# Kernel tuning notes

Measured on AMD Instinct MI355X. Metric: run time of the kernel, lower is better.

The kernel has to match this reference:

```python
import jax, jax.numpy as jnp
import numpy as np

E, K, H, I = 8, 2, 768, 1152  # experts, top_k, hidden, intermediate
T = 4096  # total tokens


def setup_inputs() -> dict:
    key = jax.random.key(0)
    ks = jax.random.split(key, 6)
    return {
        "x": jax.random.normal(ks[0], (T, H), jnp.float32),
        "gate_w": jax.random.normal(ks[1], (E, H), jnp.float32) * 0.02,
        "correction_bias": jnp.zeros((E,), jnp.float32),
        "Wi": jax.random.normal(ks[2], (E, H, 2 * I), jnp.float32) * 0.02,
        "Wo": jax.random.normal(ks[3], (E, I, H), jnp.float32) * 0.02,
        "shared_Wi": jax.random.normal(ks[4], (2 * I, H), jnp.float32) * 0.02,
        "shared_Wo": jax.random.normal(ks[5], (H, I), jnp.float32) * 0.02,
    }


def reference(x, gate_w, correction_bias, Wi, Wo, shared_Wi, shared_Wo):
    # ---- shared SwiGLU expert (dropout=0 in eval) ----
    sh = x @ shared_Wi.T                      # (T, 2I)
    s_in, s_gate = sh[:, :I], sh[:, I:]
    shared_out = (jax.nn.silu(s_in) * s_gate) @ shared_Wo.T  # (T, H)

    # ---- sigmoid top-k router with bias correction ----
    logits = jax.nn.sigmoid(x @ gate_w.T)     # (T, E)
    sel = logits + correction_bias
    _, indices = jax.lax.top_k(sel, K)        # (T, K)
    weights = jnp.take_along_axis(logits, indices, axis=-1)  # bias-free scores
    weights = weights / jnp.sum(weights, axis=-1, keepdims=True)

    # combine weight per (expert, token): cw[e, t] = sum_k weights[t,k]*[indices[t,k]==e]
    one_hot = jax.nn.one_hot(indices, E, dtype=x.dtype)      # (T, K, E)
    cw = jnp.einsum("tke,tk->et", one_hot, weights)          # (E, T)

    # ---- experts: SwiGLU per expert, weighted scatter-combine ----
    h = jnp.einsum("th,ehf->etf", x, Wi)      # (E, T, 2I)
    proj, gate = h[..., :I], h[..., I:]
    act = jax.nn.silu(gate) * proj            # (E, T, I)
    act = act * cw[:, :, None]                # fold combine weights before Wo
    expert_out = jnp.einsum("eti,eih->th", act, Wo)          # (T, H)

    return expert_out + shared_out
```

## Files before the change

### kernel.cpp

```cpp
#include <hip/hip_runtime.h>
#include <stdint.h>

#define E_  8
#define H_  768
#define I_  1152
#define T_  4096
#define F2_ (2*I_)
#define RBMAX 104

typedef unsigned short u16;
typedef __attribute__((ext_vector_type(8))) __bf16 bf16x8;
typedef __attribute__((ext_vector_type(8))) unsigned short u16x8;
typedef __attribute__((ext_vector_type(4))) float floatx4;

typedef const void __attribute__((address_space(1))) as1_void;
typedef void __attribute__((address_space(3))) as3_void;

__device__ __forceinline__ void gld16(void* lds, const void* g) {
  __builtin_amdgcn_global_load_lds((as1_void*)g, (as3_void*)lds, 16, 0, 0);
}

__device__ __forceinline__ u16 f2bf(float f) {
  union { float f; unsigned int i; } v; v.f = f;
  unsigned int r = v.i + 0x7FFF + ((v.i >> 16) & 1);
  return (u16)(r >> 16);
}


__device__ __forceinline__ void pack_direct(const float* __restrict__ src,
                                            u16* __restrict__ dst, int N, int K,
                                            int n0, int k0, int tid) {
  int n = tid & 63, kc2 = tid >> 6;
  int KT = K >> 5;
  #pragma unroll
  for (int pass = 0; pass < 2; pass++) {
    int kc = kc2 + pass * 4;
    int k  = k0 + kc * 8;
    const float* sp = src + (long)(n0 + n) * K + k;
    float4 v0 = *(const float4*)sp;
    float4 v1 = *(const float4*)(sp + 4);
    u16x8 u;
    u[0]=f2bf(v0.x); u[1]=f2bf(v0.y); u[2]=f2bf(v0.z); u[3]=f2bf(v0.w);
    u[4]=f2bf(v1.x); u[5]=f2bf(v1.y); u[6]=f2bf(v1.z); u[7]=f2bf(v1.w);
    long p = (long)((n0 + n) >> 4) * KT + (k >> 5);
    int lane = (n & 15) | ((kc & 3) << 4);
    *(u16x8*)(dst + (p * 64 + lane) * 8) = u;
  }
}

__device__ __forceinline__ void pack_transpose(const float* __restrict__ src,
                                               u16* __restrict__ dst, int N, int K,
                                               int n0, int k0, float (*tile)[65], int tid) {
  int cc = tid & 63, rr = tid >> 6;
  #pragma unroll
  for (int p = 0; p < 16; p++)
    tile[rr + p * 4][cc] = src[(long)(k0 + rr + p * 4) * N + n0 + cc];
  __syncthreads();
  int n = tid & 63, kc2 = tid >> 6;
  int KT = K >> 5;
  #pragma unroll
  for (int pass = 0; pass < 2; pass++) {
    int kc = kc2 + pass * 4;
    int k  = k0 + kc * 8;
    u16x8 u;
    #pragma unroll
    for (int e = 0; e < 8; e++) u[e] = f2bf(tile[kc * 8 + e][n]);
    long p = (long)((n0 + n) >> 4) * KT + (k >> 5);
    int lane = (n & 15) | ((kc & 3) << 4);
    *(u16x8*)(dst + (p * 64 + lane) * 8) = u;
  }
}

__global__ void prep_kernel(const float* __restrict__ x, const float* __restrict__ gw,
                            const float* __restrict__ bias,
                            int* __restrict__ top2e, float* __restrict__ top2w,
                            u16* __restrict__ xb,
                            const float* __restrict__ sWi, u16* __restrict__ sWip,
                            const float* __restrict__ sWo, u16* __restrict__ sWop,
                            const float* __restrict__ Wi, u16* __restrict__ Wip,
                            const float* __restrict__ Wo, u16* __restrict__ Wop) {
  __shared__ float tile[64][65];
  int b = blockIdx.x, tid = threadIdx.x;
  if (b < 1024) {
    int t    = b * 4 + (tid >> 6);
    int lane = tid & 63;
    float acc[E_];
    #pragma unroll
    for (int e = 0; e < E_; e++) acc[e] = 0.f;
    #pragma unroll
    for (int i = 0; i < H_ / 256; i++) {
      int c = i * 256 + lane * 4;
      float4 xv = *(const float4*)(x + (long)t * H_ + c);
      ushort4 u;
      u.x = f2bf(xv.x); u.y = f2bf(xv.y); u.z = f2bf(xv.z); u.w = f2bf(xv.w);
      *(ushort4*)(xb + (long)t * H_ + c) = u;
      #pragma unroll
      for (int e = 0; e < E_; e++) {
        float4 g = *(const float4*)(gw + e * H_ + c);
        acc[e] += xv.x * g.x + xv.y * g.y + xv.z * g.z + xv.w * g.w;
      }
    }
    #pragma unroll
    for (int e = 0; e < E_; e++) {
      #pragma unroll
      for (int s = 32; s > 0; s >>= 1) acc[e] += __shfl_xor(acc[e], s);
    }
    if (lane == 0) {
      float logits[E_], sel[E_];
      #pragma unroll
      for (int e = 0; e < E_; e++) {
        logits[e] = 1.f / (1.f + expf(-acc[e]));
        sel[e]    = logits[e] + bias[e];
      }
      int i0 = 0;
      #pragma unroll
      for (int e = 1; e < E_; e++) if (sel[e] > sel[i0]) i0 = e;
      int i1 = (i0 == 0) ? 1 : 0;
      #pragma unroll
      for (int e = 0; e < E_; e++) if (e != i0 && sel[e] > sel[i1]) i1 = e;
      float w0 = logits[i0], w1 = logits[i1], s = w0 + w1;
      top2e[t * 2 + 0] = i0;  top2w[t * 2 + 0] = w0 / s;
      top2e[t * 2 + 1] = i1;  top2w[t * 2 + 1] = w1 / s;
    }
  } else if (b < 1456) {
    int idx = b - 1024;
    int bx = idx % 36, by = idx / 36;
    pack_direct(sWi, sWip, F2_, H_, bx * 64, by * 64, tid);
  } else if (b < 1672) {
    int idx = b - 1456;
    int bx = idx % 12, by = idx / 12;
    pack_direct(sWo, sWop, H_, I_, bx * 64, by * 64, tid);
  } else if (b < 5128) {
    int idx = b - 1672;
    int e = idx / 432, rem = idx % 432;
    int bx = rem % 36, by = rem / 36;
    pack_transpose(Wi + (long)e * H_ * F2_, Wip + (long)e * F2_ * H_,
                   F2_, H_, bx * 64, by * 64, tile, tid);
  } else {
    int idx = b - 5128;
    int e = idx / 216, rem = idx % 216;
    int bx = rem % 12, by = rem / 12;
    pack_transpose(Wo + (long)e * I_ * H_, Wop + (long)e * H_ * I_,
                   H_, I_, bx * 64, by * 64, tile, tid);
  }
}

__global__ void build_lists(const int* __restrict__ top2e, const float* __restrict__ top2w,
                            int* __restrict__ counts, int* __restrict__ offs,
                            int* __restrict__ list, float* __restrict__ wlist,
                            int* __restrict__ pos, int* __restrict__ rbc) {
  __shared__ int scnt[4][E_];
  __shared__ int sq[4];
  __shared__ int soffs[E_];
  int e = blockIdx.x;
  int tid = threadIdx.x, w = tid >> 6, lane = tid & 63;
  const int Q = (2 * T_) / 4;

  int c8[E_];
  #pragma unroll
  for (int q = 0; q < E_; q++) c8[q] = 0;
  for (int i = tid; i < 2 * T_; i += 256) {
    int v = top2e[i];
    #pragma unroll
    for (int q = 0; q < E_; q++) c8[q] += (v == q);
  }
  int qstart = w * Q;
  int ce = 0;
  for (int i = qstart + lane; i < qstart + Q; i += 64) ce += (top2e[i] == e);
  #pragma unroll
  for (int q = 0; q < E_; q++)
    #pragma unroll
    for (int s = 32; s > 0; s >>= 1) c8[q] += __shfl_xor(c8[q], s);
  #pragma unroll
  for (int s = 32; s > 0; s >>= 1) ce += __shfl_xor(ce, s);
  if (lane == 0) {
    #pragma unroll
    for (int q = 0; q < E_; q++) scnt[w][q] = c8[q];
    sq[w] = ce;
  }
  __syncthreads();
  if (tid == 0) {
    int s = 0, rb = 0;
    if (e == 0) rbc[0] = 0;
    #pragma unroll
    for (int q = 0; q < E_; q++) {
      int tot = scnt[0][q] + scnt[1][q] + scnt[2][q] + scnt[3][q];
      soffs[q] = s;
      if (e == 0) {
        counts[q] = tot; offs[q] = s;
        rb += (tot + 127) / 128;
        rbc[q + 1] = rb;
      }
      s += tot;
    }
    if (e == 0) {
      counts[8] = T_; offs[8] = 2 * T_;
      rbc[9] = rb + T_ / 128;
    }
  }
  __syncthreads();
  int base = soffs[e];
  #pragma unroll
  for (int w2 = 0; w2 < 4; w2++) if (w2 < w) base += sq[w2];
  unsigned long long lt = (lane == 63) ? (~0ull >> 1) : ((1ull << lane) - 1);
  for (int i0 = qstart; i0 < qstart + Q; i0 += 64) {
    int s = i0 + lane;
    bool m = (top2e[s] == e);
    unsigned long long mask = __ballot(m);
    if (m) {
      int p = base + __popcll(mask & lt);
      list[p]  = s >> 1;
      wlist[p] = top2w[s];
      pos[s]   = p;
    }
    base += __popcll(mask);
  }
  for (int t = e * (T_ / 8) + tid; t < (e + 1) * (T_ / 8); t += 256) {
    list[2 * T_ + t]  = t;
    wlist[2 * T_ + t] = 1.f;
  }
}

__global__ __launch_bounds__(256, 2)
void gemm_act_all(const u16* __restrict__ A, const u16* __restrict__ Wip,
                  const u16* __restrict__ sWip, u16* __restrict__ act,
                  const int* __restrict__ list, const float* __restrict__ wlist,
                  const int* __restrict__ counts, const int* __restrict__ offsets,
                  const int* __restrict__ rbc) {
  __shared__ __align__(16) u16 As[128 * 64];

  int id = blockIdx.x;
  int r = id / 24, xblk = id - r * 24;
  if (xblk >= 18) return;
  if (r >= rbc[9]) return;
  int z = 0;
  while (r >= rbc[z + 1]) z++;
  int y = r - rbc[z];
  int cnt = counts[z], off = offsets[z];
  int row0 = y * 128;
  const u16* Bp = (z == 8) ? sWip : (Wip + (long)z * F2_ * H_);
  int n0 = xblk * 64;

  int tid  = threadIdx.x;
  int lane = tid & 63, wv = tid >> 6;
  int wr   = wv >> 1, wc = wv & 1;
  int half = lane & 15, quad = lane >> 4;

  int rA  = tid >> 3;
  int lc8 = ((tid & 7) ^ (rA & 7)) * 8;
  const u16* ap[4];
  #pragma unroll
  for (int n = 0; n < 4; n++) {
    int rr = min(row0 + rA + n * 32, cnt - 1);
    ap[n] = A + (long)list[off + rr] * H_ + lc8;
  }
  const int KT1 = H_ / 32;
  const u16* bb[2][2];
  #pragma unroll
  for (int h = 0; h < 2; h++)
    #pragma unroll
    for (int j = 0; j < 2; j++) {
      long nt = (h * I_ + n0 + wc * 32 + j * 16) >> 4;
      bb[h][j] = Bp + (nt * KT1 * 64 + lane) * 8;
    }

  floatx4 acc[2][4][2];
  #pragma unroll
  for (int q = 0; q < 2; q++)
    #pragma unroll
    for (int i = 0; i < 4; i++)
      #pragma unroll
      for (int j = 0; j < 2; j++) acc[q][i][j] = (floatx4)0.f;

  for (int k0 = 0; k0 < H_; k0 += 64) {
    int kt = k0 >> 5;
    bf16x8 bq[2][2][2];
    #pragma unroll
    for (int kk = 0; kk < 2; kk++)
      #pragma unroll
      for (int h = 0; h < 2; h++)
        #pragma unroll
        for (int j = 0; j < 2; j++)
          bq[kk][h][j] = *(const bf16x8*)(bb[h][j] + (kt + kk) * 512);
    if (k0) __syncthreads();
    #pragma unroll
    for (int n = 0; n < 4; n++) gld16(As + (n * 256 + tid) * 8, ap[n] + k0);
    __syncthreads();
    #pragma unroll
    for (int kk = 0; kk < 2; kk++) {
      int cs = ((kk * 4 + quad) ^ (half & 7)) * 8;
      bf16x8 a[4];
      #pragma unroll
      for (int i = 0; i < 4; i++)
        a[i] = *(const bf16x8*)(As + (wr * 64 + i * 16 + half) * 64 + cs);
      #pragma unroll
      for (int i = 0; i < 4; i++)
        #pragma unroll
        for (int q = 0; q < 2; q++)
          #pragma unroll
          for (int j = 0; j < 2; j++)
            acc[q][i][j] = __builtin_amdgcn_mfma_f32_16x16x32_bf16(a[i], bq[kk][q][j], acc[q][i][j], 0, 0, 0);
    }
  }

  bool sh = (z == 8);
  #pragma unroll
  for (int i = 0; i < 4; i++) {
    #pragma unroll
    for (int rr = 0; rr < 4; rr++) {
      int g = row0 + wr * 64 + i * 16 + quad * 4 + rr;
      if (g < cnt) {
        float w = wlist[off + g];
        #pragma unroll
        for (int j = 0; j < 2; j++) {
          float va = acc[0][i][j][rr];
          float vb = acc[1][i][j][rr];
          float zz = sh ? va : vb;
          float o  = sh ? vb : va;
          float sg = zz / (1.f + expf(-zz));
          float v  = sg * o * w;
          int col  = n0 + wc * 32 + j * 16 + half;
          act[(long)(off + g) * I_ + col] = f2bf(v);
        }
      }
    }
  }
}

__global__ __launch_bounds__(256, 2)
void gemm_out_all(const u16* __restrict__ A, const u16* __restrict__ Wop,
                  const u16* __restrict__ sWop, float* __restrict__ out,
                  float* __restrict__ eobuf,
                  const int* __restrict__ counts, const int* __restrict__ offsets,
                  const int* __restrict__ rbc) {
  __shared__ __align__(16) u16 As[128 * 64];

  int id = blockIdx.x;
  int r = id >> 3, xblk = id & 7;
  if (xblk >= 6) return;
  if (r >= rbc[9]) return;
  int z = 0;
  while (r >= rbc[z + 1]) z++;
  int y = r - rbc[z];
  int cnt = counts[z], off = offsets[z];
  int row0 = y * 128;
  const u16* Bp = (z == 8) ? sWop : (Wop + (long)z * H_ * I_);
  int n0 = xblk * 128;

  int tid  = threadIdx.x;
  int lane = tid & 63, wv = tid >> 6;
  int wr   = wv >> 1, wc = wv & 1;
  int half = lane & 15, quad = lane >> 4;

  int rA  = tid >> 3;
  int lc8 = ((tid & 7) ^ (rA & 7)) * 8;
  const u16* ap[4];
  #pragma unroll
  for (int n = 0; n < 4; n++) {
    long rr = off + min(row0 + rA + n * 32, cnt - 1);
    ap[n] = A + rr * I_ + lc8;
  }
  const int KT2 = I_ / 32;
  const u16* bb[4];
  #pragma unroll
  for (int j = 0; j < 4; j++) {
    long nt = (n0 + wc * 64 + j * 16) >> 4;
    bb[j] = Bp + (nt * KT2 * 64 + lane) * 8;
  }

  floatx4 acc[4][4];
  #pragma unroll
  for (int i = 0; i < 4; i++)
    #pragma unroll
    for (int j = 0; j < 4; j++) acc[i][j] = (floatx4)0.f;

  for (int k0 = 0; k0 < I_; k0 += 64) {
    int kt = k0 >> 5;
    bf16x8 bq[2][4];
    #pragma unroll
    for (int kk = 0; kk < 2; kk++)
      #pragma unroll
      for (int j = 0; j < 4; j++)
        bq[kk][j] = *(const bf16x8*)(bb[j] + (kt + kk) * 512);
    if (k0) __syncthreads();
    #pragma unroll
    for (int n = 0; n < 4; n++) gld16(As + (n * 256 + tid) * 8, ap[n] + k0);
    __syncthreads();
    #pragma unroll
    for (int kk = 0; kk < 2; kk++) {
      int cs = ((kk * 4 + quad) ^ (half & 7)) * 8;
      bf16x8 a[4];
      #pragma unroll
      for (int i = 0; i < 4; i++)
        a[i] = *(const bf16x8*)(As + (wr * 64 + i * 16 + half) * 64 + cs);
      #pragma unroll
      for (int i = 0; i < 4; i++)
        #pragma unroll
        for (int j = 0; j < 4; j++)
          acc[i][j] = __builtin_amdgcn_mfma_f32_16x16x32_bf16(a[i], bq[kk][j], acc[i][j], 0, 0, 0);
    }
  }

  bool sh = (z == 8);
  #pragma unroll
  for (int i = 0; i < 4; i++) {
    #pragma unroll
    for (int rr = 0; rr < 4; rr++) {
      int g = row0 + wr * 64 + i * 16 + quad * 4 + rr;
      if (g < cnt) {
        float* orow = sh ? (out + (long)g * H_) : (eobuf + (long)(off + g) * H_);
        #pragma unroll
        for (int j = 0; j < 4; j++) {
          int col = n0 + wc * 64 + j * 16 + half;
          orow[col] = acc[i][j][rr];
        }
      }
    }
  }
}

__global__ void final_reduce(float* __restrict__ out, const float* __restrict__ eobuf,
                             const int* __restrict__ pos) {
  int gid = blockIdx.x * 256 + threadIdx.x;
  int t = gid / (H_ / 4), c = (gid % (H_ / 4)) * 4;
  int p0 = pos[t * 2], p1 = pos[t * 2 + 1];
  float4 a = *(const float4*)(out   + (long)t  * H_ + c);
  float4 b = *(const float4*)(eobuf + (long)p0 * H_ + c);
  float4 d = *(const float4*)(eobuf + (long)p1 * H_ + c);
  a.x += b.x + d.x; a.y += b.y + d.y; a.z += b.z + d.z; a.w += b.w + d.w;
  *(float4*)(out + (long)t * H_ + c) = a;
}

extern "C" void kernel_launch(void* const* d_in, const int* in_sizes, int n_in,
                              void* d_out, int out_size, void* d_ws, size_t ws_size,
                              hipStream_t stream) {
  const float* x      = (const float*)d_in[0];
  const float* gate_w = (const float*)d_in[1];
  const float* bias   = (const float*)d_in[2];
  const float* Wi     = (const float*)d_in[3];
  const float* Wo     = (const float*)d_in[4];
  const float* sWi    = (const float*)d_in[5];
  const float* sWo    = (const float*)d_in[6];
  float* out          = (float*)d_out;

  char* ws = (char*)d_ws;
  size_t o = 0;
  auto alloc = [&](size_t bytes) -> void* {
    o = (o + 255) & ~(size_t)255;
    void* p = ws + o;
    o += bytes;
    return p;
  };
  u16*   xb    = (u16*)  alloc((size_t)T_ * H_ * 2);
  u16*   sWip  = (u16*)  alloc((size_t)F2_ * H_ * 2);
  u16*   sWop  = (u16*)  alloc((size_t)H_ * I_ * 2);
  u16*   Wip   = (u16*)  alloc((size_t)E_ * F2_ * H_ * 2);
  u16*   Wop   = (u16*)  alloc((size_t)E_ * H_ * I_ * 2);
  u16*   act   = (u16*)  alloc((size_t)3 * T_ * I_ * 2);
  int*   top2e = (int*)  alloc((size_t)T_ * 2 * 4);
  float* top2w = (float*)alloc((size_t)T_ * 2 * 4);
  int*   count = (int*)  alloc(16 * 4);
  int*   offs  = (int*)  alloc(16 * 4);
  int*   list  = (int*)  alloc((size_t)3 * T_ * 4);
  float* wlist = (float*)alloc((size_t)3 * T_ * 4);
  int*   pos   = (int*)  alloc((size_t)2 * T_ * 4);
  int*   rbc   = (int*)  alloc(16 * 4);
  float* eobuf = (float*)Wip;

  prep_kernel<<<6856, 256, 0, stream>>>(x, gate_w, bias, top2e, top2w, xb,
                                        sWi, sWip, sWo, sWop, Wi, Wip, Wo, Wop);
  build_lists<<<E_, 256, 0, stream>>>(top2e, top2w, count, offs, list, wlist, pos, rbc);

  gemm_act_all<<<RBMAX * 24, 256, 0, stream>>>(xb, Wip, sWip, act, list, wlist,
                                               count, offs, rbc);
  gemm_out_all<<<RBMAX * 8, 256, 0, stream>>>(act, Wop, sWop, out, eobuf,
                                              count, offs, rbc);
  final_reduce<<<(T_ * (H_ / 4)) / 256, 256, 0, stream>>>(out, eobuf, pos);
}
```

Before: 312.4 us.

## Stage weight tiles through LDS via direct global-to-LDS loads and raise occupancy

```diff
diff --git a/kernel.cpp b/kernel.cpp
--- a/kernel.cpp
+++ b/kernel.cpp
@@ -221,13 +221,14 @@
   }
 }
 
-__global__ __launch_bounds__(256, 2)
+__global__ __launch_bounds__(256, 4)
 void gemm_act_all(const u16* __restrict__ A, const u16* __restrict__ Wip,
                   const u16* __restrict__ sWip, u16* __restrict__ act,
                   const int* __restrict__ list, const float* __restrict__ wlist,
                   const int* __restrict__ counts, const int* __restrict__ offsets,
                   const int* __restrict__ rbc) {
   __shared__ __align__(16) u16 As[128 * 64];
+  __shared__ __align__(16) u16 Bs[16 * 512];
 
   int id = blockIdx.x;
   int r = id / 24, xblk = id - r * 24;
@@ -255,14 +256,16 @@
     ap[n] = A + (long)list[off + rr] * H_ + lc8;
   }
   const int KT1 = H_ / 32;
-  const u16* bb[2][2];
-  #pragma unroll
-  for (int h = 0; h < 2; h++)
-    #pragma unroll
-    for (int j = 0; j < 2; j++) {
-      long nt = (h * I_ + n0 + wc * 32 + j * 16) >> 4;
-      bb[h][j] = Bp + (nt * KT1 * 64 + lane) * 8;
-    }
+  const u16* bsrc[4];
+  u16* bdst[4];
+  #pragma unroll
+  for (int i = 0; i < 4; i++) {
+    int p  = wv * 4 + i;
+    int kk = p >> 3, h = (p >> 2) & 1, jn = p & 3;
+    long nt = ((h * I_ + n0) >> 4) + jn;
+    bsrc[i] = Bp + ((nt * KT1 + kk) * 64 + lane) * 8;
+    bdst[i] = Bs + p * 512 + lane * 8;
+  }
 
   floatx4 acc[2][4][2];
   #pragma unroll
@@ -273,33 +276,31 @@
       for (int j = 0; j < 2; j++) acc[q][i][j] = (floatx4)0.f;
 
   for (int k0 = 0; k0 < H_; k0 += 64) {
-    int kt = k0 >> 5;
-    bf16x8 bq[2][2][2];
-    #pragma unroll
-    for (int kk = 0; kk < 2; kk++)
+    if (k0) __syncthreads();
+    #pragma unroll
+    for (int n = 0; n < 4; n++) gld16(As + (n * 256 + tid) * 8, ap[n] + k0);
+    #pragma unroll
+    for (int i = 0; i < 4; i++) gld16(bdst[i], bsrc[i] + (long)k0 * 16);
+    __syncthreads();
+    #pragma unroll
+    for (int kk = 0; kk < 2; kk++) {
+      int cs = ((kk * 4 + quad) ^ (half & 7)) * 8;
+      bf16x8 a[4], bq[2][2];
+      #pragma unroll
+      for (int i = 0; i < 4; i++)
+        a[i] = *(const bf16x8*)(As + (wr * 64 + i * 16 + half) * 64 + cs);
       #pragma unroll
       for (int h = 0; h < 2; h++)
         #pragma unroll
         for (int j = 0; j < 2; j++)
-          bq[kk][h][j] = *(const bf16x8*)(bb[h][j] + (kt + kk) * 512);
-    if (k0) __syncthreads();
-    #pragma unroll
-    for (int n = 0; n < 4; n++) gld16(As + (n * 256 + tid) * 8, ap[n] + k0);
-    __syncthreads();
-    #pragma unroll
-    for (int kk = 0; kk < 2; kk++) {
-      int cs = ((kk * 4 + quad) ^ (half & 7)) * 8;
-      bf16x8 a[4];
-      #pragma unroll
-      for (int i = 0; i < 4; i++)
-        a[i] = *(const bf16x8*)(As + (wr * 64 + i * 16 + half) * 64 + cs);
+          bq[h][j] = *(const bf16x8*)(Bs + ((kk * 8 + h * 4 + wc * 2 + j) * 64 + lane) * 8);
       #pragma unroll
       for (int i = 0; i < 4; i++)
         #pragma unroll
         for (int q = 0; q < 2; q++)
           #pragma unroll
           for (int j = 0; j < 2; j++)
-            acc[q][i][j] = __builtin_amdgcn_mfma_f32_16x16x32_bf16(a[i], bq[kk][q][j], acc[q][i][j], 0, 0, 0);
+            acc[q][i][j] = __builtin_amdgcn_mfma_f32_16x16x32_bf16(a[i], bq[q][j], acc[q][i][j], 0, 0, 0);
     }
   }
 
@@ -327,13 +328,14 @@
   }
 }
 
-__global__ __launch_bounds__(256, 2)
+__global__ __launch_bounds__(256, 4)
 void gemm_out_all(const u16* __restrict__ A, const u16* __restrict__ Wop,
                   const u16* __restrict__ sWop, float* __restrict__ out,
                   float* __restrict__ eobuf,
                   const int* __restrict__ counts, const int* __restrict__ offsets,
                   const int* __restrict__ rbc) {
   __shared__ __align__(16) u16 As[128 * 64];
+  __shared__ __align__(16) u16 Bs[16 * 512];
 
   int id = blockIdx.x;
   int r = id >> 3, xblk = id & 7;
@@ -361,11 +363,15 @@
     ap[n] = A + rr * I_ + lc8;
   }
   const int KT2 = I_ / 32;
-  const u16* bb[4];
-  #pragma unroll
-  for (int j = 0; j < 4; j++) {
-    long nt = (n0 + wc * 64 + j * 16) >> 4;
-    bb[j] = Bp + (nt * KT2 * 64 + lane) * 8;
+  const u16* bsrc[4];
+  u16* bdst[4];
+  #pragma unroll
+  for (int i = 0; i < 4; i++) {
+    int p  = wv * 4 + i;
+    int kk = p >> 3, jn = p & 7;
+    long nt = (n0 >> 4) + jn;
+    bsrc[i] = Bp + ((nt * KT2 + kk) * 64 + lane) * 8;
+    bdst[i] = Bs + p * 512 + lane * 8;
   }
 
   floatx4 acc[4][4];
@@ -375,29 +381,27 @@
     for (int j = 0; j < 4; j++) acc[i][j] = (floatx4)0.f;
 
   for (int k0 = 0; k0 < I_; k0 += 64) {
-    int kt = k0 >> 5;
-    bf16x8 bq[2][4];
-    #pragma unroll
-    for (int kk = 0; kk < 2; kk++)
-      #pragma unroll
-      for (int j = 0; j < 4; j++)
-        bq[kk][j] = *(const bf16x8*)(bb[j] + (kt + kk) * 512);
     if (k0) __syncthreads();
     #pragma unroll
     for (int n = 0; n < 4; n++) gld16(As + (n * 256 + tid) * 8, ap[n] + k0);
+    #pragma unroll
+    for (int i = 0; i < 4; i++) gld16(bdst[i], bsrc[i] + (long)k0 * 16);
     __syncthreads();
     #pragma unroll
     for (int kk = 0; kk < 2; kk++) {
       int cs = ((kk * 4 + quad) ^ (half & 7)) * 8;
-      bf16x8 a[4];
+      bf16x8 a[4], b[4];
       #pragma unroll
       for (int i = 0; i < 4; i++)
         a[i] = *(const bf16x8*)(As + (wr * 64 + i * 16 + half) * 64 + cs);
+      #pragma unroll
+      for (int j = 0; j < 4; j++)
+        b[j] = *(const bf16x8*)(Bs + ((kk * 8 + wc * 4 + j) * 64 + lane) * 8);
       #pragma unroll
       for (int i = 0; i < 4; i++)
         #pragma unroll
         for (int j = 0; j < 4; j++)
-          acc[i][j] = __builtin_amdgcn_mfma_f32_16x16x32_bf16(a[i], bq[kk][j], acc[i][j], 0, 0, 0);
+          acc[i][j] = __builtin_amdgcn_mfma_f32_16x16x32_bf16(a[i], b[j], acc[i][j], 0, 0, 0);
     }
   }
 
```

New measurement: 305.3 us. -2.3%, faster.
